# Optimization experiments

Measured on AMD Instinct MI355X. Metric: run time of the kernel, lower is better.

The kernel has to match this reference:

```python
import jax, jax.numpy as jnp
import numpy as np

EPS = 1e-9

def setup_inputs() -> dict:
    key = jax.random.key(0)
    k1, k2, k3, k4 = jax.random.split(key, 4)
    B, D, M, R, C = 1024, 16, 4, 4096, 64
    x = jax.random.normal(k1, (B, D), dtype=jnp.float32)
    centers = jax.random.normal(k2, (D, M), dtype=jnp.float32)
    widths = jnp.ones((D, M), dtype=jnp.float32)
    consequents = jax.random.normal(k3, (R, D + 1, C), dtype=jnp.float32)
    rules = jax.random.randint(k4, (R, D), 0, M)  # rule -> MF index per input dim
    return {"x": x, "centers": centers, "widths": widths,
            "consequents": consequents, "rules": rules}

def reference(x, centers, widths, consequents, rules):
    B, D = x.shape
    # Gaussian membership values: [B, D, M]
    mfs = jnp.exp(-(x[:, :, None] - centers[None]) ** 2 / (2.0 * widths[None] ** 2)) + EPS
    # Gather per-rule MFs: rule_mfs[b, d, r] = mfs[b, d, rules[r, d]] -> [B, D, R]
    rule_mfs = jnp.take_along_axis(mfs, rules.T[None, :, :], axis=2)
    # Product firing strengths and normalization: [B, R]
    fs = jnp.prod(rule_mfs, axis=1)
    nfs = fs / (fs.sum(axis=1, keepdims=True) + EPS)
    # Extended input with bias: [B, D+1]
    x_ext = jnp.concatenate([x, jnp.ones((B, 1), dtype=x.dtype)], axis=1)
    # NOTE: faithful to the original torch code: 'bi,rjc->brc' has no shared
    # contraction index, so it sums x_ext over i and consequents over j.
    rule_out = jnp.einsum('br,brc->bc', nfs,
                          jnp.einsum('bi,rjc->brc', x_ext, consequents))
    return rule_out, nfs, x_ext
```

## Files before the change

kernel.cpp:

```cpp
#include <hip/hip_runtime.h>
#include <hip/hip_bf16.h>

typedef __attribute__((ext_vector_type(8))) short short8;
typedef __attribute__((ext_vector_type(4))) float floatx4;
typedef unsigned int u32;
typedef unsigned short u16;

#define NB 1024
#define ND 16
#define NM 4
#define NR 4096
#define NC 64
#define EPSF 1e-9f
#define KSPLIT 8

__device__ inline u16 f2bf(float f) {
    u32 u;
    __builtin_memcpy(&u, &f, 4);
    u32 lsb = (u >> 16) & 1;
    u += 0x7fffu + lsb;
    return (u16)(u >> 16);
}

__device__ inline void gload16(u16* lds, const u16* g) {
    __builtin_amdgcn_global_load_lds((const __attribute__((address_space(1))) u32*)g,
                                     (__attribute__((address_space(3))) u32*)lds, 16, 0, 0);
}

__global__ __launch_bounds__(256) void k_prep(const float* __restrict__ cons,
                                              const int* __restrict__ rules,
                                              u16* __restrict__ s_consT,
                                              u32* __restrict__ packed) {
    __shared__ u16 tile[64][72];
    int rbase = blockIdx.x * 64;
    int tid = threadIdx.x;
    int c = tid & 63;
#pragma unroll
    for (int rr = tid >> 6; rr < 64; rr += 4) {
        int r = rbase + rr;
        const float* p = cons + (size_t)r * (ND + 1) * NC + c;
        float s = 0.f;
#pragma unroll
        for (int j = 0; j < ND + 1; ++j) s += p[j * NC];
        tile[rr][c] = f2bf(s);
    }
    if (tid < 64) {
        const int* q = rules + (size_t)(rbase + tid) * ND;
        u32 pk = 0;
#pragma unroll
        for (int d = 0; d < ND; ++d) pk |= ((u32)(q[d] & 3)) << (2 * d);
        packed[rbase + tid] = pk;
    }
    __syncthreads();
#pragma unroll
    for (int pass = 0; pass < 2; ++pass) {
        int cc = pass * 32 + (tid >> 3);
        int r0 = (tid & 7) * 8;
        short8 v;
#pragma unroll
        for (int e = 0; e < 8; ++e) v[e] = (short)tile[r0 + e][cc];
        *(short8*)(s_consT + (size_t)cc * NR + rbase + r0) = v;
    }
}

__global__ __launch_bounds__(256) void k_fs(const float* __restrict__ x,
                                            const float* __restrict__ centers,
                                            const float* __restrict__ widths,
                                            const u32* __restrict__ packed,
                                            float* __restrict__ out_nfs,
                                            u16* __restrict__ nfs_bf,
                                            float* __restrict__ out_xe,
                                            float* __restrict__ sx) {
    __shared__ float xv[16];
    __shared__ float mftab[64];
    __shared__ float gtab[1024];
    __shared__ float fsbuf[4096];
    __shared__ float wred[4];
    __shared__ float s_inv;
    int b = blockIdx.x;
    int tid = threadIdx.x;
    if (tid < 16) {
        float raw = x[b * 16 + tid];
        xv[tid] = raw;
        out_xe[b * 17 + tid] = raw;
    }
    if (tid == 16) out_xe[b * 17 + 16] = 1.0f;
    __syncthreads();
    if (tid < 64) {
        float diff = xv[tid >> 2] - centers[tid];
        float w = widths[tid];
        mftab[tid] = __expf(-diff * diff / (2.f * w * w)) + EPSF;
    }
    if (tid == 0) {
        float s = 1.f;
        for (int i = 0; i < 16; ++i) s += xv[i];
        sx[b] = s;
    }
    __syncthreads();
    for (int idx = tid; idx < 1024; idx += 256) {
        int g = idx >> 8, i = idx & 255;
        const float* mf = mftab + g * 16;
        gtab[idx] = mf[0 + (i & 3)] * mf[4 + ((i >> 2) & 3)] *
                    mf[8 + ((i >> 4) & 3)] * mf[12 + ((i >> 6) & 3)];
    }
    __syncthreads();
    float lsum = 0.f;
    for (int r = tid; r < NR; r += 256) {
        u32 p = packed[r];
        float f = gtab[p & 255] * gtab[256 + ((p >> 8) & 255)] *
                  gtab[512 + ((p >> 16) & 255)] * gtab[768 + (p >> 24)];
        fsbuf[r] = f;
        lsum += f;
    }
    for (int off = 32; off; off >>= 1) lsum += __shfl_down(lsum, off, 64);
    if ((tid & 63) == 0) wred[tid >> 6] = lsum;
    __syncthreads();
    if (tid == 0) s_inv = 1.f / (wred[0] + wred[1] + wred[2] + wred[3] + EPSF);
    __syncthreads();
    float inv = s_inv;
    float* on = out_nfs + (size_t)b * NR;
    u16* ob = nfs_bf + (size_t)b * NR;
    for (int r = tid; r < NR; r += 256) {
        float v = fsbuf[r] * inv;
        on[r] = v;
        ob[r] = f2bf(v);
    }
}

__global__ __launch_bounds__(256) void k_gemm(const u16* __restrict__ nfs,
                                              const u16* __restrict__ s_consT,
                                              float* __restrict__ part) {
    __shared__ __align__(16) u16 Abuf[2][128 * 32];
    __shared__ __align__(16) u16 Bbuf[2][64 * 32];
    int rt = blockIdx.x;
    int ks = blockIdx.y;
    int tid = threadIdx.x;
    int wid = tid >> 6, lane = tid & 63;
    int rowbase = rt * 128;
    int kbase0 = ks * (NR / KSPLIT);
    floatx4 acc[2][4] = {};

    auto stage = [&](int buf, int kb) {
#pragma unroll
        for (int q = 0; q < 2; ++q) {
            int chunk = wid * 2 + q;
            int row = rowbase + chunk * 16 + (lane >> 2);
            const u16* g = nfs + (size_t)row * NR + kb + (lane & 3) * 8;
            gload16(&Abuf[buf][chunk * 512 + lane * 8], g);
        }
        int c = wid * 16 + (lane >> 2);
        const u16* g = s_consT + (size_t)c * NR + kb + (lane & 3) * 8;
        gload16(&Bbuf[buf][wid * 512 + lane * 8], g);
    };

    stage(0, kbase0);
    asm volatile("s_waitcnt vmcnt(0)" ::: "memory");
    __syncthreads();
    int cur = 0;
    const int NT = (NR / KSPLIT) / 32;
    for (int t = 0; t < NT; ++t) {
        if (t + 1 < NT) stage(cur ^ 1, kbase0 + (t + 1) * 32);
        short8 af[2], bfv[4];
#pragma unroll
        for (int rb = 0; rb < 2; ++rb)
            af[rb] = *(const short8*)&Abuf[cur][(wid * 32 + rb * 16 + (lane & 15)) * 32 + (lane >> 4) * 8];
#pragma unroll
        for (int cb = 0; cb < 4; ++cb)
            bfv[cb] = *(const short8*)&Bbuf[cur][(cb * 16 + (lane & 15)) * 32 + (lane >> 4) * 8];
#pragma unroll
        for (int rb = 0; rb < 2; ++rb)
#pragma unroll
            for (int cb = 0; cb < 4; ++cb)
                acc[rb][cb] = __builtin_amdgcn_mfma_f32_16x16x32_bf16(af[rb], bfv[cb], acc[rb][cb], 0, 0, 0);
        asm volatile("s_waitcnt vmcnt(0)" ::: "memory");
        __syncthreads();
        cur ^= 1;
    }
#pragma unroll
    for (int rb = 0; rb < 2; ++rb)
#pragma unroll
        for (int cb = 0; cb < 4; ++cb)
#pragma unroll
            for (int reg = 0; reg < 4; ++reg) {
                int row = rowbase + wid * 32 + rb * 16 + (lane >> 4) * 4 + reg;
                int col = cb * 16 + (lane & 15);
                part[(size_t)ks * (NB * NC) + (size_t)row * NC + col] = acc[rb][cb][reg];
            }
}

__global__ __launch_bounds__(256) void k_out(const float* __restrict__ part,
                                             const float* __restrict__ sx,
                                             float* __restrict__ out0) {
    int t = blockIdx.x * 256 + threadIdx.x;
    if (t >= NB * NC) return;
    float a = 0.f;
#pragma unroll
    for (int ks = 0; ks < KSPLIT; ++ks) a += part[(size_t)ks * (NB * NC) + t];
    out0[t] = a * sx[t >> 6];
}

extern "C" void kernel_launch(void* const* d_in, const int* in_sizes, int n_in,
                              void* d_out, int out_size, void* d_ws, size_t ws_size,
                              hipStream_t stream) {
    const float* x = (const float*)d_in[0];
    const float* centers = (const float*)d_in[1];
    const float* widths = (const float*)d_in[2];
    const float* cons = (const float*)d_in[3];
    const int* rules = (const int*)d_in[4];

    float* out = (float*)d_out;
    float* out_rule = out;
    float* out_nfs = out + NB * NC;
    float* out_xe = out + NB * NC + NB * NR;

    char* ws = (char*)d_ws;
    u16* s_consT = (u16*)ws;
    u32* packed = (u32*)(ws + (512 << 10));
    float* sx = (float*)(ws + (512 << 10) + (16 << 10));
    float* part = (float*)(ws + (512 << 10) + (20 << 10));
    u16* nfs_bf = (u16*)(ws + (512 << 10) + (20 << 10) + (NB * NC * KSPLIT * 4));

    k_prep<<<NR / 64, 256, 0, stream>>>(cons, rules, s_consT, packed);
    k_fs<<<NB, 256, 0, stream>>>(x, centers, widths, packed, out_nfs, nfs_bf, out_xe, sx);
    k_gemm<<<dim3(NB / 128, KSPLIT), 256, 0, stream>>>(nfs_bf, s_consT, part);
    k_out<<<(NB * NC + 255) / 256, 256, 0, stream>>>(part, sx, out_rule);
}
```

Baseline: 38.42 us.

## Raise grid parallelism in prep and GEMM, vectorize firing-strength kernel memory ops

k_prep now processes 16 rules per block instead of 64, launching four times as many blocks. k_fs reads the packed rules, writes fsbuf and stores both outputs with 4-wide vector accesses instead of scalar ones. k_gemm drops the LDS double-buffered staging and loads MFMA operands straight from global memory, using 64-row tiles to double the block count. These changes target low occupancy and scalar memory traffic, at the cost of redundant global reads of B across waves and the loss of async LDS prefetch.

Result: faster. 33.34 us (-13.2%).

```diff
diff --git a/kernel.cpp b/kernel.cpp
--- a/kernel.cpp
+++ b/kernel.cpp
@@ -2,7 +2,9 @@
 #include <hip/hip_bf16.h>
 
 typedef __attribute__((ext_vector_type(8))) short short8;
+typedef __attribute__((ext_vector_type(4))) short short4v;
 typedef __attribute__((ext_vector_type(4))) float floatx4;
+typedef __attribute__((ext_vector_type(4))) unsigned int uintx4;
 typedef unsigned int u32;
 typedef unsigned short u16;
 
@@ -22,29 +24,26 @@
     return (u16)(u >> 16);
 }
 
-__device__ inline void gload16(u16* lds, const u16* g) {
-    __builtin_amdgcn_global_load_lds((const __attribute__((address_space(1))) u32*)g,
-                                     (__attribute__((address_space(3))) u32*)lds, 16, 0, 0);
-}
-
 __global__ __launch_bounds__(256) void k_prep(const float* __restrict__ cons,
                                               const int* __restrict__ rules,
                                               u16* __restrict__ s_consT,
                                               u32* __restrict__ packed) {
-    __shared__ u16 tile[64][72];
-    int rbase = blockIdx.x * 64;
+    __shared__ u16 tile[16][68];
+    int rbase = blockIdx.x * 16;
     int tid = threadIdx.x;
     int c = tid & 63;
-#pragma unroll
-    for (int rr = tid >> 6; rr < 64; rr += 4) {
-        int r = rbase + rr;
-        const float* p = cons + (size_t)r * (ND + 1) * NC + c;
-        float s = 0.f;
-#pragma unroll
-        for (int j = 0; j < ND + 1; ++j) s += p[j * NC];
-        tile[rr][c] = f2bf(s);
-    }
-    if (tid < 64) {
+    {
+        int rr = tid >> 6;
+#pragma unroll
+        for (int it = 0; it < 4; ++it, rr += 4) {
+            const float* p = cons + (size_t)(rbase + rr) * (ND + 1) * NC + c;
+            float s = 0.f;
+#pragma unroll
+            for (int j = 0; j < ND + 1; ++j) s += p[j * NC];
+            tile[rr][c] = f2bf(s);
+        }
+    }
+    if (tid < 16) {
         const int* q = rules + (size_t)(rbase + tid) * ND;
         u32 pk = 0;
 #pragma unroll
@@ -52,14 +51,13 @@
         packed[rbase + tid] = pk;
     }
     __syncthreads();
-#pragma unroll
-    for (int pass = 0; pass < 2; ++pass) {
-        int cc = pass * 32 + (tid >> 3);
-        int r0 = (tid & 7) * 8;
-        short8 v;
-#pragma unroll
-        for (int e = 0; e < 8; ++e) v[e] = (short)tile[r0 + e][cc];
-        *(short8*)(s_consT + (size_t)cc * NR + rbase + r0) = v;
+    {
+        int cc = tid >> 2;
+        int r0 = (tid & 3) * 4;
+        short4v v;
+#pragma unroll
+        for (int e = 0; e < 4; ++e) v[e] = (short)tile[r0 + e][cc];
+        *(short4v*)(s_consT + (size_t)cc * NR + rbase + r0) = v;
     }
 }
 
@@ -105,12 +103,19 @@
     }
     __syncthreads();
     float lsum = 0.f;
-    for (int r = tid; r < NR; r += 256) {
-        u32 p = packed[r];
-        float f = gtab[p & 255] * gtab[256 + ((p >> 8) & 255)] *
-                  gtab[512 + ((p >> 16) & 255)] * gtab[768 + (p >> 24)];
-        fsbuf[r] = f;
-        lsum += f;
+#pragma unroll
+    for (int it = 0; it < 4; ++it) {
+        int r = it * 1024 + tid * 4;
+        uintx4 p = *(const uintx4*)(packed + r);
+        floatx4 f;
+#pragma unroll
+        for (int e = 0; e < 4; ++e) {
+            u32 pk = p[e];
+            f[e] = gtab[pk & 255] * gtab[256 + ((pk >> 8) & 255)] *
+                   gtab[512 + ((pk >> 16) & 255)] * gtab[768 + (pk >> 24)];
+            lsum += f[e];
+        }
+        *(floatx4*)(fsbuf + r) = f;
     }
     for (int off = 32; off; off >>= 1) lsum += __shfl_down(lsum, off, 64);
     if ((tid & 63) == 0) wred[tid >> 6] = lsum;
@@ -120,72 +125,53 @@
     float inv = s_inv;
     float* on = out_nfs + (size_t)b * NR;
     u16* ob = nfs_bf + (size_t)b * NR;
-    for (int r = tid; r < NR; r += 256) {
-        float v = fsbuf[r] * inv;
-        on[r] = v;
-        ob[r] = f2bf(v);
+#pragma unroll
+    for (int it = 0; it < 4; ++it) {
+        int r = it * 1024 + tid * 4;
+        floatx4 f = *(const floatx4*)(fsbuf + r);
+        floatx4 v;
+        short4v bv;
+#pragma unroll
+        for (int e = 0; e < 4; ++e) {
+            v[e] = f[e] * inv;
+            bv[e] = (short)f2bf(v[e]);
+        }
+        *(floatx4*)(on + r) = v;
+        *(short4v*)(ob + r) = bv;
     }
 }
 
 __global__ __launch_bounds__(256) void k_gemm(const u16* __restrict__ nfs,
                                               const u16* __restrict__ s_consT,
                                               float* __restrict__ part) {
-    __shared__ __align__(16) u16 Abuf[2][128 * 32];
-    __shared__ __align__(16) u16 Bbuf[2][64 * 32];
     int rt = blockIdx.x;
     int ks = blockIdx.y;
     int tid = threadIdx.x;
     int wid = tid >> 6, lane = tid & 63;
-    int rowbase = rt * 128;
-    int kbase0 = ks * (NR / KSPLIT);
-    floatx4 acc[2][4] = {};
-
-    auto stage = [&](int buf, int kb) {
-#pragma unroll
-        for (int q = 0; q < 2; ++q) {
-            int chunk = wid * 2 + q;
-            int row = rowbase + chunk * 16 + (lane >> 2);
-            const u16* g = nfs + (size_t)row * NR + kb + (lane & 3) * 8;
-            gload16(&Abuf[buf][chunk * 512 + lane * 8], g);
-        }
-        int c = wid * 16 + (lane >> 2);
-        const u16* g = s_consT + (size_t)c * NR + kb + (lane & 3) * 8;
-        gload16(&Bbuf[buf][wid * 512 + lane * 8], g);
-    };
-
-    stage(0, kbase0);
-    asm volatile("s_waitcnt vmcnt(0)" ::: "memory");
-    __syncthreads();
-    int cur = 0;
-    const int NT = (NR / KSPLIT) / 32;
-    for (int t = 0; t < NT; ++t) {
-        if (t + 1 < NT) stage(cur ^ 1, kbase0 + (t + 1) * 32);
-        short8 af[2], bfv[4];
-#pragma unroll
-        for (int rb = 0; rb < 2; ++rb)
-            af[rb] = *(const short8*)&Abuf[cur][(wid * 32 + rb * 16 + (lane & 15)) * 32 + (lane >> 4) * 8];
-#pragma unroll
-        for (int cb = 0; cb < 4; ++cb)
-            bfv[cb] = *(const short8*)&Bbuf[cur][(cb * 16 + (lane & 15)) * 32 + (lane >> 4) * 8];
-#pragma unroll
-        for (int rb = 0; rb < 2; ++rb)
-#pragma unroll
-            for (int cb = 0; cb < 4; ++cb)
-                acc[rb][cb] = __builtin_amdgcn_mfma_f32_16x16x32_bf16(af[rb], bfv[cb], acc[rb][cb], 0, 0, 0);
-        asm volatile("s_waitcnt vmcnt(0)" ::: "memory");
-        __syncthreads();
-        cur ^= 1;
-    }
-#pragma unroll
-    for (int rb = 0; rb < 2; ++rb)
-#pragma unroll
-        for (int cb = 0; cb < 4; ++cb)
-#pragma unroll
-            for (int reg = 0; reg < 4; ++reg) {
-                int row = rowbase + wid * 32 + rb * 16 + (lane >> 4) * 4 + reg;
-                int col = cb * 16 + (lane & 15);
-                part[(size_t)ks * (NB * NC) + (size_t)row * NC + col] = acc[rb][cb][reg];
-            }
+    int arow = rt * 64 + wid * 16 + (lane & 15);
+    int klane = (lane >> 4) * 8;
+    int kbase = ks * (NR / KSPLIT);
+    const u16* aptr = nfs + (size_t)arow * NR + kbase + klane;
+    const u16* bptr = s_consT + (size_t)(lane & 15) * NR + kbase + klane;
+    floatx4 acc[4] = {};
+#pragma unroll 4
+    for (int t = 0; t < 16; ++t) {
+        short8 af = *(const short8*)(aptr + t * 32);
+#pragma unroll
+        for (int cb = 0; cb < 4; ++cb) {
+            short8 bf = *(const short8*)(bptr + (size_t)cb * 16 * NR + t * 32);
+            acc[cb] = __builtin_amdgcn_mfma_f32_16x16x32_bf16(af, bf, acc[cb], 0, 0, 0);
+        }
+    }
+    float* po = part + (size_t)ks * (NB * NC);
+#pragma unroll
+    for (int cb = 0; cb < 4; ++cb)
+#pragma unroll
+        for (int reg = 0; reg < 4; ++reg) {
+            int row = rt * 64 + wid * 16 + (lane >> 4) * 4 + reg;
+            int col = cb * 16 + (lane & 15);
+            po[(size_t)row * NC + col] = acc[cb][reg];
+        }
 }
 
 __global__ __launch_bounds__(256) void k_out(const float* __restrict__ part,
@@ -220,8 +206,8 @@
     float* part = (float*)(ws + (512 << 10) + (20 << 10));
     u16* nfs_bf = (u16*)(ws + (512 << 10) + (20 << 10) + (NB * NC * KSPLIT * 4));
 
-    k_prep<<<NR / 64, 256, 0, stream>>>(cons, rules, s_consT, packed);
+    k_prep<<<NR / 16, 256, 0, stream>>>(cons, rules, s_consT, packed);
     k_fs<<<NB, 256, 0, stream>>>(x, centers, widths, packed, out_nfs, nfs_bf, out_xe, sx);
-    k_gemm<<<dim3(NB / 128, KSPLIT), 256, 0, stream>>>(nfs_bf, s_consT, part);
+    k_gemm<<<dim3(NB / 64, KSPLIT), 256, 0, stream>>>(nfs_bf, s_consT, part);
     k_out<<<(NB * NC + 255) / 256, 256, 0, stream>>>(part, sx, out_rule);
 }
```
